# Optimization experiments

Hardware: AMD Instinct MI355X
Metric: run time of the kernel (lower is better)

Reference implementation:

```python
import jax, jax.numpy as jnp
import numpy as np

BATCH, INPUT_DIM, OUTPUT_DIM = 8192, 256, 256
NUM_CENTERS, ORDER = 512, 8


def setup_inputs() -> dict:
    key = jax.random.key(0)
    kx, kc, kw = jax.random.split(key, 3)
    x = jax.random.normal(kx, (BATCH, INPUT_DIM), dtype=jnp.float32)
    # xavier_uniform for centers [num_centers, input_dim]
    lim_c = float(np.sqrt(6.0 / (NUM_CENTERS + INPUT_DIM)))
    centers = jax.random.uniform(kc, (NUM_CENTERS, INPUT_DIM), jnp.float32, -lim_c, lim_c)
    # xavier_uniform for weights [num_centers, order+1, output_dim]
    # torch treats fan_in = (order+1)*output_dim? For 3D, fan_in = size(1)*size(2)... use dims 1,2 receptive field convention:
    fan_in = (ORDER + 1) * OUTPUT_DIM
    fan_out = NUM_CENTERS * OUTPUT_DIM
    lim_w = float(np.sqrt(6.0 / (fan_in + fan_out)))
    weights = jax.random.uniform(kw, (NUM_CENTERS, ORDER + 1, OUTPUT_DIM), jnp.float32, -lim_w, lim_w)
    return {"x": x, "centers": centers, "weights": weights}


def _legendre_basis(t, order):
    """Stack P_0..P_order evaluated at t via the three-term recurrence.
    (n+1) P_{n+1}(t) = (2n+1) t P_n(t) - n P_{n-1}(t)."""
    polys = [jnp.ones_like(t), t]
    for n in range(1, order):
        polys.append(((2.0 * n + 1.0) * t * polys[-1] - n * polys[-2]) / (n + 1.0))
    return jnp.stack(polys[: order + 1], axis=-1)  # [..., order+1]


def reference(x, centers, weights):
    # pairwise euclidean distances [batch, num_centers] via the gram trick
    x2 = jnp.sum(x * x, axis=1, keepdims=True)             # [b, 1]
    c2 = jnp.sum(centers * centers, axis=1)[None, :]       # [1, c]
    d2 = x2 + c2 - 2.0 * (x @ centers.T)
    distances = jnp.sqrt(jnp.maximum(d2, 0.0))
    dmin, dmax = distances.min(), distances.max()
    t = 2.0 * (distances - dmin) / (dmax - dmin) - 1.0     # [b, c] in [-1, 1]
    # torch code round-trips through numpy -> basis is detached from the graph
    t = jax.lax.stop_gradient(t)
    order = weights.shape[1] - 1
    basis = _legendre_basis(t, order)                      # [b, c, order+1]
    # einsum 'bcn,cnf->bcf' followed by sum over c == single contraction
    return jnp.einsum('bcn,cnf->bf', basis, weights)       # [b, output_dim]
```

## Files before the change

kernel.cpp:

```cpp
#include <hip/hip_runtime.h>
#include <hip/hip_bf16.h>
#include <stdint.h>

#define BATCH   8192
#define IN_DIM  256
#define OUT_DIM 256
#define NC      512
#define NORD    9
#define KTOT    (NC * NORD)

#define OFF_MM  0u
#define OFF_X2  256u
#define OFF_C2  (OFF_X2 + BATCH * 4u)
#define OFF_D   35072u
#define OFF_WT  (OFF_D + (size_t)BATCH * NC * 4u)
#define OFF_G   (OFF_WT + (size_t)OUT_DIM * KTOT * 2u)

typedef __bf16 bf16x8 __attribute__((ext_vector_type(8)));
typedef float  f32x4  __attribute__((ext_vector_type(4)));

__device__ inline unsigned short f2bf(float f) {
  unsigned u = __float_as_uint(f);
  return (unsigned short)((u + 0x7FFFu + ((u >> 16) & 1u)) >> 16);
}

__device__ inline void gload_lds16(const void* g, void* l) {
  __builtin_amdgcn_global_load_lds(
      (const __attribute__((address_space(1))) unsigned int*)(uintptr_t)g,
      (__attribute__((address_space(3))) unsigned int*)(uint32_t)(uintptr_t)l,
      16, 0, 0);
}

__global__ void k_init_mm(unsigned* mm) {
  mm[0] = 0x7F800000u;
  mm[1] = 0u;
}

__global__ __launch_bounds__(64) void k_rowsq(const float* __restrict__ src,
                                              float* __restrict__ dst) {
  const int row  = blockIdx.x;
  const int lane = threadIdx.x;
  const float4 v = *(const float4*)(src + (size_t)row * IN_DIM + lane * 4);
  float s = v.x * v.x + v.y * v.y + v.z * v.z + v.w * v.w;
  #pragma unroll
  for (int m = 1; m < 64; m <<= 1) s += __shfl_xor(s, m, 64);
  if (lane == 0) dst[row] = s;
}

__global__ __launch_bounds__(256) void k_dist(const float* __restrict__ x,
                                              const float* __restrict__ cen,
                                              const float* __restrict__ x2,
                                              const float* __restrict__ c2,
                                              float* __restrict__ d,
                                              unsigned* __restrict__ mm) {
  __shared__ float As[64][36];
  __shared__ float Bs[64][36];
  const int tid = threadIdx.x;
  const int bm0 = blockIdx.x * 64, bc0 = blockIdx.y * 64;
  float acc[4][4] = {};
  for (int k0 = 0; k0 < IN_DIM; k0 += 32) {
    __syncthreads();
    #pragma unroll
    for (int it = 0; it < 2; ++it) {
      const int row = (tid >> 3) + it * 32;
      const int c4  = (tid & 7) * 4;
      *(float4*)&As[row][c4] = *(const float4*)(x   + (size_t)(bm0 + row) * IN_DIM + k0 + c4);
      *(float4*)&Bs[row][c4] = *(const float4*)(cen + (size_t)(bc0 + row) * IN_DIM + k0 + c4);
    }
    __syncthreads();
    const int r0 = tid >> 4, c0 = tid & 15;
    #pragma unroll
    for (int k4 = 0; k4 < 32; k4 += 4) {
      float4 a[4], b[4];
      #pragma unroll
      for (int i = 0; i < 4; ++i) a[i] = *(const float4*)&As[r0 + 16 * i][k4];
      #pragma unroll
      for (int j = 0; j < 4; ++j) b[j] = *(const float4*)&Bs[c0 + 16 * j][k4];
      #pragma unroll
      for (int i = 0; i < 4; ++i)
        #pragma unroll
        for (int j = 0; j < 4; ++j)
          acc[i][j] += a[i].x * b[j].x + a[i].y * b[j].y +
                       a[i].z * b[j].z + a[i].w * b[j].w;
    }
  }
  const int r0 = tid >> 4, c0 = tid & 15;
  float lmin = 1e30f, lmax = -1e30f;
  #pragma unroll
  for (int i = 0; i < 4; ++i) {
    const float xs = x2[bm0 + r0 + 16 * i];
    #pragma unroll
    for (int j = 0; j < 4; ++j) {
      float d2 = xs + c2[bc0 + c0 + 16 * j] - 2.0f * acc[i][j];
      float dd = sqrtf(fmaxf(d2, 0.0f));
      d[(size_t)(bm0 + r0 + 16 * i) * NC + bc0 + c0 + 16 * j] = dd;
      lmin = fminf(lmin, dd);
      lmax = fmaxf(lmax, dd);
    }
  }
  #pragma unroll
  for (int m = 1; m < 64; m <<= 1) {
    lmin = fminf(lmin, __shfl_xor(lmin, m, 64));
    lmax = fmaxf(lmax, __shfl_xor(lmax, m, 64));
  }
  __shared__ float rmin[4], rmax[4];
  const int wid = tid >> 6, lane = tid & 63;
  if (lane == 0) { rmin[wid] = lmin; rmax[wid] = lmax; }
  __syncthreads();
  if (tid == 0) {
    float m0 = fminf(fminf(rmin[0], rmin[1]), fminf(rmin[2], rmin[3]));
    float m1 = fmaxf(fmaxf(rmax[0], rmax[1]), fmaxf(rmax[2], rmax[3]));
    atomicMin(mm + 0, __float_as_uint(m0));
    atomicMax(mm + 1, __float_as_uint(m1));
  }
}

__global__ __launch_bounds__(256) void k_prepw(const float* __restrict__ w,
                                               unsigned short* __restrict__ wt) {
  __shared__ float t[64][65];
  const int k0 = blockIdx.x * 64, f0 = blockIdx.y * 64;
  const int tid = threadIdx.x;
  const int c = tid & 63, rb = tid >> 6;
  #pragma unroll
  for (int i = 0; i < 16; ++i) {
    const int r = rb + 4 * i;
    t[r][c] = w[(size_t)(k0 + r) * OUT_DIM + f0 + c];
  }
  __syncthreads();
  #pragma unroll
  for (int i = 0; i < 16; ++i) {
    const int r = rb + 4 * i;
    wt[(size_t)(f0 + r) * KTOT + k0 + c] = f2bf(t[c][r]);
  }
}

__global__ __launch_bounds__(256) void k_basis(const float* __restrict__ d,
                                               const unsigned* __restrict__ mm,
                                               unsigned short* __restrict__ G) {
  const int gid = blockIdx.x * 256 + threadIdx.x;
  const float dmin = __uint_as_float(mm[0]);
  const float dmax = __uint_as_float(mm[1]);
  const float inv  = 2.0f / (dmax - dmin);
  const float tt   = (d[gid] - dmin) * inv - 1.0f;
  unsigned short o[NORD];
  float p0 = 1.0f, p1 = tt;
  o[0] = f2bf(p0);
  o[1] = f2bf(p1);
  #pragma unroll
  for (int n = 1; n <= 7; ++n) {
    const float p2 = ((2.0f * n + 1.0f) * tt * p1 - (float)n * p0) * (1.0f / (n + 1));
    o[n + 1] = f2bf(p2);
    p0 = p1;
    p1 = p2;
  }
  unsigned short* gp = G + (size_t)gid * NORD;
  #pragma unroll
  for (int n = 0; n < NORD; ++n) gp[n] = o[n];
}

__global__ __launch_bounds__(256) void k_zero(float4* __restrict__ out) {
  out[(size_t)blockIdx.x * 256 + threadIdx.x] = float4{0.f, 0.f, 0.f, 0.f};
}

__global__ __launch_bounds__(256) void k_gemm(const unsigned short* __restrict__ G,
                                              const unsigned short* __restrict__ Wt,
                                              float* __restrict__ out) {
  __shared__ unsigned short As[128 * 64];
  __shared__ unsigned short Bs[64 * 64];
  const int tid  = threadIdx.x;
  const int bm0  = blockIdx.x * 128;
  const int bn0  = blockIdx.y * 64;
  const int kb0  = blockIdx.z * (KTOT / 2);
  const int lane = tid & 63;
  const int wid  = tid >> 6;
  const int wm = wid >> 1, wn = wid & 1;
  f32x4 acc[4][2] = {};
  const char* gA = (const char*)G;
  const char* gB = (const char*)Wt;
  char* lA = (char*)As;
  char* lB = (char*)Bs;
  for (int step = 0; step < (KTOT / 2) / 64; ++step) {
    const int k0 = kb0 + step * 64;
    __syncthreads();
    #pragma unroll
    for (int p = 0; p < 4; ++p) {
      const int flat = p * 4096 + tid * 16;
      const int row = flat >> 7, cb = flat & 127;
      const int srcb = cb ^ ((row & 7) << 4);
      gload_lds16(gA + ((size_t)(bm0 + row) * KTOT + k0) * 2 + srcb, lA + flat);
    }
    #pragma unroll
    for (int p = 0; p < 2; ++p) {
      const int flat = p * 4096 + tid * 16;
      const int row = flat >> 7, cb = flat & 127;
      const int srcb = cb ^ ((row & 7) << 4);
      gload_lds16(gB + ((size_t)(bn0 + row) * KTOT + k0) * 2 + srcb, lB + flat);
    }
    __syncthreads();
    #pragma unroll
    for (int ks = 0; ks < 2; ++ks) {
      bf16x8 af[4], bfr[2];
      const int kb = ks * 64 + (lane >> 4) * 16;
      #pragma unroll
      for (int m = 0; m < 4; ++m) {
        const int row = wm * 64 + m * 16 + (lane & 15);
        af[m] = *(const bf16x8*)(lA + row * 128 + (kb ^ ((row & 7) << 4)));
      }
      #pragma unroll
      for (int n = 0; n < 2; ++n) {
        const int row = wn * 32 + n * 16 + (lane & 15);
        bfr[n] = *(const bf16x8*)(lB + row * 128 + (kb ^ ((row & 7) << 4)));
      }
      #pragma unroll
      for (int m = 0; m < 4; ++m)
        #pragma unroll
        for (int n = 0; n < 2; ++n)
          acc[m][n] = __builtin_amdgcn_mfma_f32_16x16x32_bf16(af[m], bfr[n], acc[m][n], 0, 0, 0);
    }
  }
  #pragma unroll
  for (int m = 0; m < 4; ++m) {
    const int row0 = bm0 + wm * 64 + m * 16 + (lane >> 4) * 4;
    #pragma unroll
    for (int n = 0; n < 2; ++n) {
      const int col = bn0 + wn * 32 + n * 16 + (lane & 15);
      #pragma unroll
      for (int j = 0; j < 4; ++j)
        atomicAdd(out + (size_t)(row0 + j) * OUT_DIM + col, acc[m][n][j]);
    }
  }
}

extern "C" void kernel_launch(void* const* d_in, const int* in_sizes, int n_in,
                              void* d_out, int out_size, void* d_ws, size_t ws_size,
                              hipStream_t stream) {
  const float* x   = (const float*)d_in[0];
  const float* cen = (const float*)d_in[1];
  const float* w   = (const float*)d_in[2];
  float* out = (float*)d_out;
  char* ws = (char*)d_ws;

  unsigned*       mm = (unsigned*)(ws + OFF_MM);
  float*          x2 = (float*)(ws + OFF_X2);
  float*          c2 = (float*)(ws + OFF_C2);
  float*          dd = (float*)(ws + OFF_D);
  unsigned short* wt = (unsigned short*)(ws + OFF_WT);
  unsigned short* G  = (unsigned short*)(ws + OFF_G);

  k_init_mm<<<1, 1, 0, stream>>>(mm);
  k_rowsq<<<BATCH, 64, 0, stream>>>(x, x2);
  k_rowsq<<<NC, 64, 0, stream>>>(cen, c2);
  k_dist<<<dim3(BATCH / 64, NC / 64), 256, 0, stream>>>(x, cen, x2, c2, dd, mm);
  k_prepw<<<dim3(KTOT / 64, OUT_DIM / 64), 256, 0, stream>>>(w, wt);
  k_basis<<<(BATCH * NC) / 256, 256, 0, stream>>>(dd, mm, G);
  k_zero<<<(BATCH * OUT_DIM) / (256 * 4), 256, 0, stream>>>((float4*)out);
  k_gemm<<<dim3(BATCH / 128, OUT_DIM / 64, 2), 256, 0, stream>>>(G, wt, out);
}
```

Measured before the change: 186.0 us.

## Fuse Legendre basis into MFMA GEMM and split-bf16 MFMA distance kernel

Replaces the fp32 SIMT distance GEMM with a bf16 MFMA GEMM that uses a hi/lo split of x and centers (K extended to 768) to keep roughly fp32-level accuracy. The Legendre basis is now computed in registers inside the output GEMM, with weights reordered by polynomial order. This removes the large basis buffer write/read, the zeroing kernel and the split-K atomics. The cost is more per-block LDS (72KB), which limits occupancy, and recomputing the recurrence in every output-column block.

```diff
diff --git a/kernel.cpp b/kernel.cpp
--- a/kernel.cpp
+++ b/kernel.cpp
@@ -8,13 +8,15 @@
 #define NC      512
 #define NORD    9
 #define KTOT    (NC * NORD)
+#define KE      768
 
 #define OFF_MM  0u
 #define OFF_X2  256u
-#define OFF_C2  (OFF_X2 + BATCH * 4u)
-#define OFF_D   35072u
-#define OFF_WT  (OFF_D + (size_t)BATCH * NC * 4u)
-#define OFF_G   (OFF_WT + (size_t)OUT_DIM * KTOT * 2u)
+#define OFF_C2  33024u
+#define OFF_AE  35072u
+#define OFF_BE  12617984u
+#define OFF_WT  13404416u
+#define OFF_D   15763712u
 
 typedef __bf16 bf16x8 __attribute__((ext_vector_type(8)));
 typedef float  f32x4  __attribute__((ext_vector_type(4)));
@@ -22,6 +24,9 @@
 __device__ inline unsigned short f2bf(float f) {
   unsigned u = __float_as_uint(f);
   return (unsigned short)((u + 0x7FFFu + ((u >> 16) & 1u)) >> 16);
+}
+__device__ inline float bf2f(unsigned short h) {
+  return __uint_as_float(((unsigned)h) << 16);
 }
 
 __device__ inline void gload_lds16(const void* g, void* l) {
@@ -36,66 +41,123 @@
   mm[1] = 0u;
 }
 
-__global__ __launch_bounds__(64) void k_rowsq(const float* __restrict__ src,
-                                              float* __restrict__ dst) {
+__global__ __launch_bounds__(64) void k_prep(const float* __restrict__ src,
+                                             unsigned short* __restrict__ dst,
+                                             float* __restrict__ sq,
+                                             int off_h0, int off_h1, int off_l) {
   const int row  = blockIdx.x;
   const int lane = threadIdx.x;
   const float4 v = *(const float4*)(src + (size_t)row * IN_DIM + lane * 4);
   float s = v.x * v.x + v.y * v.y + v.z * v.z + v.w * v.w;
   #pragma unroll
   for (int m = 1; m < 64; m <<= 1) s += __shfl_xor(s, m, 64);
-  if (lane == 0) dst[row] = s;
-}
-
-__global__ __launch_bounds__(256) void k_dist(const float* __restrict__ x,
-                                              const float* __restrict__ cen,
+  ushort4 h, l;
+  h.x = f2bf(v.x); h.y = f2bf(v.y); h.z = f2bf(v.z); h.w = f2bf(v.w);
+  l.x = f2bf(v.x - bf2f(h.x)); l.y = f2bf(v.y - bf2f(h.y));
+  l.z = f2bf(v.z - bf2f(h.z)); l.w = f2bf(v.w - bf2f(h.w));
+  unsigned short* rb = dst + (size_t)row * KE;
+  *(ushort4*)(rb + off_h0 + lane * 4) = h;
+  *(ushort4*)(rb + off_h1 + lane * 4) = h;
+  *(ushort4*)(rb + off_l  + lane * 4) = l;
+  if (lane == 0) sq[row] = s;
+}
+
+__global__ __launch_bounds__(256) void k_prepw(const float* __restrict__ w,
+                                               unsigned short* __restrict__ wt) {
+  __shared__ float t[64][65];
+  const int n  = blockIdx.x % 9;
+  const int cb = blockIdx.x / 9;
+  const int f0 = blockIdx.y * 64;
+  const int tid = threadIdx.x;
+  const int c = tid & 63, rb = tid >> 6;
+  #pragma unroll
+  for (int i = 0; i < 16; ++i) {
+    const int r = rb + 4 * i;
+    t[r][c] = w[((size_t)(cb * 64 + r) * 9 + n) * OUT_DIM + f0 + c];
+  }
+  __syncthreads();
+  #pragma unroll
+  for (int i = 0; i < 16; ++i) {
+    const int r = rb + 4 * i;
+    wt[(size_t)(f0 + r) * KTOT + n * 512 + cb * 64 + c] = f2bf(t[c][r]);
+  }
+}
+
+__global__ __launch_bounds__(256) void k_dist(const unsigned short* __restrict__ Ae,
+                                              const unsigned short* __restrict__ Be,
                                               const float* __restrict__ x2,
                                               const float* __restrict__ c2,
                                               float* __restrict__ d,
                                               unsigned* __restrict__ mm) {
-  __shared__ float As[64][36];
-  __shared__ float Bs[64][36];
-  const int tid = threadIdx.x;
-  const int bm0 = blockIdx.x * 64, bc0 = blockIdx.y * 64;
-  float acc[4][4] = {};
-  for (int k0 = 0; k0 < IN_DIM; k0 += 32) {
+  __shared__ unsigned short As[128 * 64];
+  __shared__ unsigned short Bs[64 * 64];
+  __shared__ float rmin[4], rmax[4];
+  const int tid  = threadIdx.x;
+  const int bm0  = blockIdx.x * 128;
+  const int bc0  = blockIdx.y * 64;
+  const int lane = tid & 63;
+  const int wid  = tid >> 6;
+  const int wm = wid >> 1, wn = wid & 1;
+  f32x4 acc[4][2] = {};
+  const char* gA = (const char*)Ae;
+  const char* gB = (const char*)Be;
+  char* lA = (char*)As;
+  char* lB = (char*)Bs;
+  for (int step = 0; step < KE / 64; ++step) {
+    const int k0 = step * 64;
     __syncthreads();
     #pragma unroll
-    for (int it = 0; it < 2; ++it) {
-      const int row = (tid >> 3) + it * 32;
-      const int c4  = (tid & 7) * 4;
-      *(float4*)&As[row][c4] = *(const float4*)(x   + (size_t)(bm0 + row) * IN_DIM + k0 + c4);
-      *(float4*)&Bs[row][c4] = *(const float4*)(cen + (size_t)(bc0 + row) * IN_DIM + k0 + c4);
+    for (int p = 0; p < 4; ++p) {
+      const int flat = p * 4096 + tid * 16;
+      const int row = flat >> 7, cb = flat & 127;
+      const int srcb = cb ^ ((row & 7) << 4);
+      gload_lds16(gA + ((size_t)(bm0 + row) * KE + k0) * 2 + srcb, lA + flat);
+    }
+    #pragma unroll
+    for (int p = 0; p < 2; ++p) {
+      const int flat = p * 4096 + tid * 16;
+      const int row = flat >> 7, cb = flat & 127;
+      const int srcb = cb ^ ((row & 7) << 4);
+      gload_lds16(gB + ((size_t)(bc0 + row) * KE + k0) * 2 + srcb, lB + flat);
     }
     __syncthreads();
-    const int r0 = tid >> 4, c0 = tid & 15;
-    #pragma unroll
-    for (int k4 = 0; k4 < 32; k4 += 4) {
-      float4 a[4], b[4];
-      #pragma unroll
-      for (int i = 0; i < 4; ++i) a[i] = *(const float4*)&As[r0 + 16 * i][k4];
-      #pragma unroll
-      for (int j = 0; j < 4; ++j) b[j] = *(const float4*)&Bs[c0 + 16 * j][k4];
-      #pragma unroll
-      for (int i = 0; i < 4; ++i)
+    #pragma unroll
+    for (int ks = 0; ks < 2; ++ks) {
+      bf16x8 af[4], bfr[2];
+      const int kb = ks * 64 + (lane >> 4) * 16;
+      #pragma unroll
+      for (int m = 0; m < 4; ++m) {
+        const int row = wm * 64 + m * 16 + (lane & 15);
+        af[m] = *(const bf16x8*)(lA + row * 128 + (kb ^ ((row & 7) << 4)));
+      }
+      #pragma unroll
+      for (int n = 0; n < 2; ++n) {
+        const int row = wn * 32 + n * 16 + (lane & 15);
+        bfr[n] = *(const bf16x8*)(lB + row * 128 + (kb ^ ((row & 7) << 4)));
+      }
+      #pragma unroll
+      for (int m = 0; m < 4; ++m)
         #pragma unroll
-        for (int j = 0; j < 4; ++j)
-          acc[i][j] += a[i].x * b[j].x + a[i].y * b[j].y +
-                       a[i].z * b[j].z + a[i].w * b[j].w;
-    }
-  }
-  const int r0 = tid >> 4, c0 = tid & 15;
+        for (int n = 0; n < 2; ++n)
+          acc[m][n] = __builtin_amdgcn_mfma_f32_16x16x32_bf16(af[m], bfr[n], acc[m][n], 0, 0, 0);
+    }
+  }
   float lmin = 1e30f, lmax = -1e30f;
   #pragma unroll
-  for (int i = 0; i < 4; ++i) {
-    const float xs = x2[bm0 + r0 + 16 * i];
+  for (int m = 0; m < 4; ++m) {
     #pragma unroll
     for (int j = 0; j < 4; ++j) {
-      float d2 = xs + c2[bc0 + c0 + 16 * j] - 2.0f * acc[i][j];
-      float dd = sqrtf(fmaxf(d2, 0.0f));
-      d[(size_t)(bm0 + r0 + 16 * i) * NC + bc0 + c0 + 16 * j] = dd;
-      lmin = fminf(lmin, dd);
-      lmax = fmaxf(lmax, dd);
+      const int row = bm0 + wm * 64 + m * 16 + (lane >> 4) * 4 + j;
+      const float xs = x2[row];
+      #pragma unroll
+      for (int n = 0; n < 2; ++n) {
+        const int col = bc0 + wn * 32 + n * 16 + (lane & 15);
+        float d2 = xs + c2[col] - 2.0f * acc[m][n][j];
+        float dd = sqrtf(fmaxf(d2, 0.0f));
+        d[(size_t)row * NC + col] = dd;
+        lmin = fminf(lmin, dd);
+        lmax = fmaxf(lmax, dd);
+      }
     }
   }
   #pragma unroll
@@ -103,8 +165,6 @@
     lmin = fminf(lmin, __shfl_xor(lmin, m, 64));
     lmax = fmaxf(lmax, __shfl_xor(lmax, m, 64));
   }
-  __shared__ float rmin[4], rmax[4];
-  const int wid = tid >> 6, lane = tid & 63;
   if (lane == 0) { rmin[wid] = lmin; rmax[wid] = lmax; }
   __syncthreads();
   if (tid == 0) {
@@ -115,118 +175,104 @@
   }
 }
 
-__global__ __launch_bounds__(256) void k_prepw(const float* __restrict__ w,
-                                               unsigned short* __restrict__ wt) {
-  __shared__ float t[64][65];
-  const int k0 = blockIdx.x * 64, f0 = blockIdx.y * 64;
-  const int tid = threadIdx.x;
-  const int c = tid & 63, rb = tid >> 6;
-  #pragma unroll
-  for (int i = 0; i < 16; ++i) {
-    const int r = rb + 4 * i;
-    t[r][c] = w[(size_t)(k0 + r) * OUT_DIM + f0 + c];
-  }
-  __syncthreads();
-  #pragma unroll
-  for (int i = 0; i < 16; ++i) {
-    const int r = rb + 4 * i;
-    wt[(size_t)(f0 + r) * KTOT + k0 + c] = f2bf(t[c][r]);
-  }
-}
-
-__global__ __launch_bounds__(256) void k_basis(const float* __restrict__ d,
+__global__ __launch_bounds__(256) void k_fused(const float* __restrict__ d,
+                                               const unsigned short* __restrict__ Wt,
                                                const unsigned* __restrict__ mm,
-                                               unsigned short* __restrict__ G) {
-  const int gid = blockIdx.x * 256 + threadIdx.x;
+                                               float* __restrict__ out) {
+  __shared__ char lB[73728];
+  const int tid  = threadIdx.x;
+  const int lane = tid & 63;
+  const int w    = tid >> 6;
+  const int bm0  = blockIdx.x * 64;
+  const int f0   = blockIdx.y * 64;
   const float dmin = __uint_as_float(mm[0]);
   const float dmax = __uint_as_float(mm[1]);
   const float inv  = 2.0f / (dmax - dmin);
-  const float tt   = (d[gid] - dmin) * inv - 1.0f;
-  unsigned short o[NORD];
-  float p0 = 1.0f, p1 = tt;
-  o[0] = f2bf(p0);
-  o[1] = f2bf(p1);
-  #pragma unroll
-  for (int n = 1; n <= 7; ++n) {
-    const float p2 = ((2.0f * n + 1.0f) * tt * p1 - (float)n * p0) * (1.0f / (n + 1));
-    o[n + 1] = f2bf(p2);
-    p0 = p1;
-    p1 = p2;
-  }
-  unsigned short* gp = G + (size_t)gid * NORD;
-  #pragma unroll
-  for (int n = 0; n < NORD; ++n) gp[n] = o[n];
-}
-
-__global__ __launch_bounds__(256) void k_zero(float4* __restrict__ out) {
-  out[(size_t)blockIdx.x * 256 + threadIdx.x] = float4{0.f, 0.f, 0.f, 0.f};
-}
-
-__global__ __launch_bounds__(256) void k_gemm(const unsigned short* __restrict__ G,
-                                              const unsigned short* __restrict__ Wt,
-                                              float* __restrict__ out) {
-  __shared__ unsigned short As[128 * 64];
-  __shared__ unsigned short Bs[64 * 64];
-  const int tid  = threadIdx.x;
-  const int bm0  = blockIdx.x * 128;
-  const int bn0  = blockIdx.y * 64;
-  const int kb0  = blockIdx.z * (KTOT / 2);
-  const int lane = tid & 63;
-  const int wid  = tid >> 6;
-  const int wm = wid >> 1, wn = wid & 1;
-  f32x4 acc[4][2] = {};
-  const char* gA = (const char*)G;
-  const char* gB = (const char*)Wt;
-  char* lA = (char*)As;
-  char* lB = (char*)Bs;
-  for (int step = 0; step < (KTOT / 2) / 64; ++step) {
-    const int k0 = kb0 + step * 64;
+  f32x4 acc[4] = {};
+  const int rowd = bm0 + w * 16 + (lane & 15);
+  const int sw   = (lane & 7) << 4;
+
+  for (int cb = 0; cb < 8; ++cb) {
     __syncthreads();
-    #pragma unroll
-    for (int p = 0; p < 4; ++p) {
+    float4 dv[4];
+    {
+      const float* dp = d + (size_t)rowd * NC + cb * 64 + (lane >> 4) * 8;
+      dv[0] = *(const float4*)(dp);
+      dv[1] = *(const float4*)(dp + 4);
+      dv[2] = *(const float4*)(dp + 32);
+      dv[3] = *(const float4*)(dp + 36);
+    }
+    #pragma unroll
+    for (int p = 0; p < 18; ++p) {
       const int flat = p * 4096 + tid * 16;
-      const int row = flat >> 7, cb = flat & 127;
-      const int srcb = cb ^ ((row & 7) << 4);
-      gload_lds16(gA + ((size_t)(bm0 + row) * KTOT + k0) * 2 + srcb, lA + flat);
-    }
-    #pragma unroll
-    for (int p = 0; p < 2; ++p) {
-      const int flat = p * 4096 + tid * 16;
-      const int row = flat >> 7, cb = flat & 127;
-      const int srcb = cb ^ ((row & 7) << 4);
-      gload_lds16(gB + ((size_t)(bn0 + row) * KTOT + k0) * 2 + srcb, lB + flat);
+      const int n    = flat >> 13;
+      const int rem  = flat & 8191;
+      const int row  = rem >> 7;
+      const int cbyt = rem & 127;
+      const int srcb = cbyt ^ ((row & 7) << 4);
+      gload_lds16((const char*)Wt + ((size_t)(f0 + row) * KTOT + n * 512 + cb * 64) * 2 + srcb,
+                  lB + flat);
+    }
+    float t_[16];
+    #pragma unroll
+    for (int q = 0; q < 4; ++q) {
+      t_[q * 4 + 0] = (dv[q].x - dmin) * inv - 1.0f;
+      t_[q * 4 + 1] = (dv[q].y - dmin) * inv - 1.0f;
+      t_[q * 4 + 2] = (dv[q].z - dmin) * inv - 1.0f;
+      t_[q * 4 + 3] = (dv[q].w - dmin) * inv - 1.0f;
     }
     __syncthreads();
-    #pragma unroll
-    for (int ks = 0; ks < 2; ++ks) {
-      bf16x8 af[4], bfr[2];
-      const int kb = ks * 64 + (lane >> 4) * 16;
-      #pragma unroll
-      for (int m = 0; m < 4; ++m) {
-        const int row = wm * 64 + m * 16 + (lane & 15);
-        af[m] = *(const bf16x8*)(lA + row * 128 + (kb ^ ((row & 7) << 4)));
+
+    #define MFMA_N(nn, af0, af1)                                                      \
+      {                                                                               \
+        _Pragma("unroll")                                                             \
+        for (int nf = 0; nf < 4; ++nf) {                                              \
+          const int rbase = (nn) * 8192 + (nf * 16 + (lane & 15)) * 128;              \
+          bf16x8 b0 = *(const bf16x8*)(lB + rbase + (((lane >> 4) * 16) ^ sw));       \
+          bf16x8 b1 = *(const bf16x8*)(lB + rbase + ((64 + (lane >> 4) * 16) ^ sw));  \
+          acc[nf] = __builtin_amdgcn_mfma_f32_16x16x32_bf16(af0, b0, acc[nf], 0, 0, 0); \
+          acc[nf] = __builtin_amdgcn_mfma_f32_16x16x32_bf16(af1, b1, acc[nf], 0, 0, 0); \
+        }                                                                             \
       }
-      #pragma unroll
-      for (int n = 0; n < 2; ++n) {
-        const int row = wn * 32 + n * 16 + (lane & 15);
-        bfr[n] = *(const bf16x8*)(lB + row * 128 + (kb ^ ((row & 7) << 4)));
-      }
-      #pragma unroll
-      for (int m = 0; m < 4; ++m)
-        #pragma unroll
-        for (int n = 0; n < 2; ++n)
-          acc[m][n] = __builtin_amdgcn_mfma_f32_16x16x32_bf16(af[m], bfr[n], acc[m][n], 0, 0, 0);
-    }
-  }
-  #pragma unroll
-  for (int m = 0; m < 4; ++m) {
-    const int row0 = bm0 + wm * 64 + m * 16 + (lane >> 4) * 4;
-    #pragma unroll
-    for (int n = 0; n < 2; ++n) {
-      const int col = bn0 + wn * 32 + n * 16 + (lane & 15);
-      #pragma unroll
-      for (int j = 0; j < 4; ++j)
-        atomicAdd(out + (size_t)(row0 + j) * OUT_DIM + col, acc[m][n][j]);
+
+    float pa[16], pb[16];
+    {
+      bf16x8 a0, a1;
+      #pragma unroll
+      for (int j = 0; j < 8; ++j) { a0[j] = (__bf16)1.0f; a1[j] = (__bf16)1.0f; }
+      MFMA_N(0, a0, a1)
+    }
+    {
+      bf16x8 a0, a1;
+      #pragma unroll
+      for (int j = 0; j < 8; ++j) { a0[j] = (__bf16)t_[j]; a1[j] = (__bf16)t_[8 + j]; }
+      MFMA_N(1, a0, a1)
+      #pragma unroll
+      for (int s = 0; s < 16; ++s) { pa[s] = 1.0f; pb[s] = t_[s]; }
+    }
+    #pragma unroll
+    for (int n = 2; n <= 8; ++n) {
+      const float an = (2.0f * n - 1.0f) / (float)n;
+      const float bn = (float)(n - 1) / (float)n;
+      float pc[16];
+      #pragma unroll
+      for (int s = 0; s < 16; ++s) pc[s] = an * t_[s] * pb[s] - bn * pa[s];
+      bf16x8 a0, a1;
+      #pragma unroll
+      for (int j = 0; j < 8; ++j) { a0[j] = (__bf16)pc[j]; a1[j] = (__bf16)pc[8 + j]; }
+      MFMA_N(n, a0, a1)
+      #pragma unroll
+      for (int s = 0; s < 16; ++s) { pa[s] = pb[s]; pb[s] = pc[s]; }
+    }
+    #undef MFMA_N
+  }
+  #pragma unroll
+  for (int nf = 0; nf < 4; ++nf) {
+    const int col = f0 + nf * 16 + (lane & 15);
+    #pragma unroll
+    for (int j = 0; j < 4; ++j) {
+      const int row = bm0 + w * 16 + (lane >> 4) * 4 + j;
+      out[(size_t)row * OUT_DIM + col] = acc[nf][j];
     }
   }
 }
@@ -243,16 +289,15 @@
   unsigned*       mm = (unsigned*)(ws + OFF_MM);
   float*          x2 = (float*)(ws + OFF_X2);
   float*          c2 = (float*)(ws + OFF_C2);
+  unsigned short* Ae = (unsigned short*)(ws + OFF_AE);
+  unsigned short* Be = (unsigned short*)(ws + OFF_BE);
+  unsigned short* wt = (unsigned short*)(ws + OFF_WT);
   float*          dd = (float*)(ws + OFF_D);
-  unsigned short* wt = (unsigned short*)(ws + OFF_WT);
-  unsigned short* G  = (unsigned short*)(ws + OFF_G);
 
   k_init_mm<<<1, 1, 0, stream>>>(mm);
-  k_rowsq<<<BATCH, 64, 0, stream>>>(x, x2);
-  k_rowsq<<<NC, 64, 0, stream>>>(cen, c2);
-  k_dist<<<dim3(BATCH / 64, NC / 64), 256, 0, stream>>>(x, cen, x2, c2, dd, mm);
-  k_prepw<<<dim3(KTOT / 64, OUT_DIM / 64), 256, 0, stream>>>(w, wt);
-  k_basis<<<(BATCH * NC) / 256, 256, 0, stream>>>(dd, mm, G);
-  k_zero<<<(BATCH * OUT_DIM) / (256 * 4), 256, 0, stream>>>((float4*)out);
-  k_gemm<<<dim3(BATCH / 128, OUT_DIM / 64, 2), 256, 0, stream>>>(G, wt, out);
-}
+  k_prep<<<BATCH, 64, 0, stream>>>(x,   Ae, x2, 0, 512, 256);
+  k_prep<<<NC,    64, 0, stream>>>(cen, Be, c2, 0, 256, 512);
+  k_prepw<<<dim3(72, 4), 256, 0, stream>>>(w, wt);
+  k_dist<<<dim3(BATCH / 128, NC / 64), 256, 0, stream>>>(Ae, Be, x2, c2, dd, mm);
+  k_fused<<<dim3(BATCH / 64, OUT_DIM / 64), 256, 0, stream>>>(dd, wt, mm, out);
+}
```

Measured after the change: 151.0 us. -18.8%, faster.
